# Kernel optimization log

Measured on AMD Instinct MI355X. Metric: run time of the kernel, lower is better.

Reference implementation:

```python
import jax, jax.numpy as jnp
import numpy as np

B, S, D = 4, 2048, 1024

def setup_inputs() -> dict:
    key = jax.random.key(0)
    k1, k2, k3, k4 = jax.random.split(key, 4)
    scale = 1.0 / np.sqrt(D)
    return {
        "x": jax.random.normal(k1, (B, S, D), dtype=jnp.float32),
        "Wq": jax.random.normal(k2, (D, D), dtype=jnp.float32) * scale,
        "Wk": jax.random.normal(k3, (D, D), dtype=jnp.float32) * scale,
        "Wv": jax.random.normal(k4, (D, D), dtype=jnp.float32) * scale,
    }

def reference(x, Wq, Wk, Wv):
    # Q, K, V projections: [B, S, D] @ [D, D]
    Q = jnp.einsum("bsd,de->bse", x, Wq)
    Kp = jnp.einsum("bsd,de->bse", x, Wk)
    V = jnp.einsum("bsd,de->bse", x, Wv)
    # scores: [B, S, S] -- NOTE: original module applies NO 1/sqrt(d) scaling
    scores = jnp.einsum("bqd,bkd->bqk", Q, Kp)
    attn = jax.nn.softmax(scores, axis=-1)
    # context: [B, S, D]
    return jnp.einsum("bqk,bkd->bqd", attn, V)
```

## Files before the change

### kernel.cpp

```cpp
#include <hip/hip_runtime.h>
#include <hip/hip_bf16.h>

#define ATT_B 4
#define ATT_S 2048
#define ATT_D 1024

#define BM 128
#define BN 128
#define BK 32

typedef __attribute__((ext_vector_type(8))) short bf16x8;
typedef __attribute__((ext_vector_type(4))) float f32x4;

__device__ inline unsigned short f2bf_rne(float f) {
  unsigned u = __float_as_uint(f);
  u += 0x7FFFu + ((u >> 16) & 1u);
  return (unsigned short)(u >> 16);
}

__device__ inline void gll16(const void* g, void* l) {
  __builtin_amdgcn_global_load_lds(
      (const __attribute__((address_space(1))) void*)g,
      (__attribute__((address_space(3))) void*)l, 16, 0, 0);
}

template<int NT, int AMODE, int OMODE>
__global__ __launch_bounds__(256, 2)
void gemm_bt(const void* __restrict__ Apv, const void* __restrict__ Alv,
             const unsigned short* __restrict__ Bh,
             const unsigned short* __restrict__ Bl,
             void* __restrict__ C0, void* __restrict__ C1,
             int K, int pitchA, int pitchB, int pitchC, int mtiles_pb,
             size_t Abstride, size_t Bbstride, size_t Cbstride)
{
  __shared__ unsigned short sAh[BM * BK];
  __shared__ unsigned short sBh[BN * BK];
  __shared__ unsigned short sAl[(NT == 3) ? BM * BK : 8];
  __shared__ unsigned short sBl[(NT == 3) ? BN * BK : 8];

  const int tid  = threadIdx.x;
  const int wave = tid >> 6;
  const int lane = tid & 63;
  const int l16  = lane & 15;
  const int lh   = lane >> 4;
  const int wm   = wave >> 1;
  const int wn   = wave & 1;

  const int bt   = blockIdx.y / mtiles_pb;
  const int ml   = blockIdx.y % mtiles_pb;
  const int row0 = ml * BM;
  const int col0 = blockIdx.x * BN;

  const unsigned short* Bhb = Bh + (size_t)bt * Bbstride;
  const unsigned short* Blb = (NT == 3) ? (Bl + (size_t)bt * Bbstride) : (const unsigned short*)nullptr;

  const unsigned short* Ahb = nullptr;
  const unsigned short* Alb = nullptr;
  const float*          Af  = nullptr;
  if (AMODE == 0) {
    Ahb = (const unsigned short*)Apv + (size_t)bt * Abstride;
    if (NT == 3) Alb = (const unsigned short*)Alv + (size_t)bt * Abstride;
  } else {
    Af = (const float*)Apv + (size_t)bt * Abstride;
  }

  f32x4 acc[4][4] = {};

  for (int k0 = 0; k0 < K; k0 += BK) {
#pragma unroll
    for (int j = 0; j < 2; ++j) {
      const int off = tid * 16 + j * 4096;
      const int r   = off >> 6;
      const int kb  = off & 63;
      const char* g = (const char*)Bhb + ((size_t)(col0 + r) * pitchB + k0) * 2 + kb;
      char* l = (char*)sBh + (wave << 10) + j * 4096;
      gll16(g, l);
    }
    if (NT == 3) {
#pragma unroll
      for (int j = 0; j < 2; ++j) {
        const int off = tid * 16 + j * 4096;
        const int r   = off >> 6;
        const int kb  = off & 63;
        const char* g = (const char*)Blb + ((size_t)(col0 + r) * pitchB + k0) * 2 + kb;
        char* l = (char*)sBl + (wave << 10) + j * 4096;
        gll16(g, l);
      }
    }

    if (AMODE == 0) {
#pragma unroll
      for (int j = 0; j < 2; ++j) {
        const int off = tid * 16 + j * 4096;
        const int r   = off >> 6;
        const int kb  = off & 63;
        const char* g = (const char*)Ahb + ((size_t)(row0 + r) * pitchA + k0) * 2 + kb;
        char* l = (char*)sAh + (wave << 10) + j * 4096;
        gll16(g, l);
      }
      if (NT == 3) {
#pragma unroll
        for (int j = 0; j < 2; ++j) {
          const int off = tid * 16 + j * 4096;
          const int r   = off >> 6;
          const int kb  = off & 63;
          const char* g = (const char*)Alb + ((size_t)(row0 + r) * pitchA + k0) * 2 + kb;
          char* l = (char*)sAl + (wave << 10) + j * 4096;
          gll16(g, l);
        }
      }
    } else {
#pragma unroll
      for (int j = 0; j < 4; ++j) {
        const int lin4 = tid + j * 256;
        const int r    = lin4 >> 3;
        const int c4   = lin4 & 7;
        const float4 v = *(const float4*)(Af + (size_t)(row0 + r) * pitchA + k0 + c4 * 4);
        const unsigned ux = __float_as_uint(v.x), uy = __float_as_uint(v.y);
        const unsigned uz = __float_as_uint(v.z), uw = __float_as_uint(v.w);
        ushort4 hi;
        hi.x = (unsigned short)(ux >> 16); hi.y = (unsigned short)(uy >> 16);
        hi.z = (unsigned short)(uz >> 16); hi.w = (unsigned short)(uw >> 16);
        *(ushort4*)&sAh[r * BK + c4 * 4] = hi;
        if (NT == 3) {
          ushort4 lo;
          lo.x = f2bf_rne(v.x - __uint_as_float(ux & 0xFFFF0000u));
          lo.y = f2bf_rne(v.y - __uint_as_float(uy & 0xFFFF0000u));
          lo.z = f2bf_rne(v.z - __uint_as_float(uz & 0xFFFF0000u));
          lo.w = f2bf_rne(v.w - __uint_as_float(uw & 0xFFFF0000u));
          *(ushort4*)&sAl[r * BK + c4 * 4] = lo;
        }
      }
    }
    __syncthreads();

    bf16x8 ah[4], bh4[4], al[4], bl4[4];
#pragma unroll
    for (int t = 0; t < 4; ++t) {
      ah[t]  = *(const bf16x8*)&sAh[(wm * 64 + t * 16 + l16) * BK + lh * 8];
      bh4[t] = *(const bf16x8*)&sBh[(wn * 64 + t * 16 + l16) * BK + lh * 8];
      if (NT == 3) {
        al[t]  = *(const bf16x8*)&sAl[(wm * 64 + t * 16 + l16) * BK + lh * 8];
        bl4[t] = *(const bf16x8*)&sBl[(wn * 64 + t * 16 + l16) * BK + lh * 8];
      }
    }
#pragma unroll
    for (int i = 0; i < 4; ++i)
#pragma unroll
      for (int j = 0; j < 4; ++j) {
        f32x4 c = acc[i][j];
        if (NT == 3) {
          c = __builtin_amdgcn_mfma_f32_16x16x32_bf16(al[i], bh4[j], c, 0, 0, 0);
          c = __builtin_amdgcn_mfma_f32_16x16x32_bf16(ah[i], bl4[j], c, 0, 0, 0);
        }
        c = __builtin_amdgcn_mfma_f32_16x16x32_bf16(ah[i], bh4[j], c, 0, 0, 0);
        acc[i][j] = c;
      }
    __syncthreads();
  }

#pragma unroll
  for (int i = 0; i < 4; ++i) {
    const int mBase = row0 + wm * 64 + i * 16 + lh * 4;
#pragma unroll
    for (int j = 0; j < 4; ++j) {
      const int n = col0 + wn * 64 + j * 16 + l16;
      if (OMODE == 0) {
        float* C = (float*)C0 + (size_t)bt * Cbstride;
#pragma unroll
        for (int r = 0; r < 4; ++r)
          C[(size_t)(mBase + r) * pitchC + n] = acc[i][j][r];
      } else if (OMODE == 1) {
        unsigned short* Ch = (unsigned short*)C0;
        unsigned short* Cl = (unsigned short*)C1;
#pragma unroll
        for (int r = 0; r < 4; ++r) {
          const float f = acc[i][j][r];
          const unsigned u = __float_as_uint(f);
          Ch[(size_t)(mBase + r) * pitchC + n] = (unsigned short)(u >> 16);
          Cl[(size_t)(mBase + r) * pitchC + n] =
              f2bf_rne(f - __uint_as_float(u & 0xFFFF0000u));
        }
      } else {
        unsigned short* Vt = (unsigned short*)C0;
        const int b2 = mBase >> 11;
        const int sr = mBase & 2047;
        ushort4 o;
        o.x = f2bf_rne(acc[i][j][0]); o.y = f2bf_rne(acc[i][j][1]);
        o.z = f2bf_rne(acc[i][j][2]); o.w = f2bf_rne(acc[i][j][3]);
        *(ushort4*)&Vt[(size_t)b2 * (1024u * 2048u) + (size_t)n * 2048 + sr] = o;
      }
    }
  }
}

__global__ __launch_bounds__(256)
void wsplit(const float* __restrict__ W, unsigned short* __restrict__ Wh,
            unsigned short* __restrict__ Wl) {
  __shared__ float t[32][33];
  const int k0 = blockIdx.x * 32;
  const int n0 = blockIdx.y * 32;
  const int tx = threadIdx.x & 31;
  const int ty = threadIdx.x >> 5;
#pragma unroll
  for (int i = 0; i < 32; i += 8)
    t[ty + i][tx] = W[(size_t)(k0 + ty + i) * 1024 + (n0 + tx)];
  __syncthreads();
#pragma unroll
  for (int i = 0; i < 32; i += 8) {
    const float f = t[tx][ty + i];
    const unsigned u = __float_as_uint(f);
    Wh[(size_t)(n0 + ty + i) * 1024 + (k0 + tx)] = (unsigned short)(u >> 16);
    Wl[(size_t)(n0 + ty + i) * 1024 + (k0 + tx)] =
        f2bf_rne(f - __uint_as_float(u & 0xFFFF0000u));
  }
}

__global__ __launch_bounds__(256)
void softmax_inplace(float* __restrict__ S) {
  const int wave = threadIdx.x >> 6;
  const int lane = threadIdx.x & 63;
  float* rp = S + ((size_t)blockIdx.x * 4 + wave) * 2048;

  float4 v[8];
#pragma unroll
  for (int i = 0; i < 8; ++i) v[i] = *(const float4*)&rp[lane * 4 + i * 256];

  float m = -1e30f;
#pragma unroll
  for (int i = 0; i < 8; ++i)
    m = fmaxf(m, fmaxf(fmaxf(v[i].x, v[i].y), fmaxf(v[i].z, v[i].w)));
#pragma unroll
  for (int s = 32; s; s >>= 1) m = fmaxf(m, __shfl_xor(m, s));

  float sum = 0.f;
#pragma unroll
  for (int i = 0; i < 8; ++i) {
    v[i].x = __expf(v[i].x - m); v[i].y = __expf(v[i].y - m);
    v[i].z = __expf(v[i].z - m); v[i].w = __expf(v[i].w - m);
    sum += (v[i].x + v[i].y) + (v[i].z + v[i].w);
  }
#pragma unroll
  for (int s = 32; s; s >>= 1) sum += __shfl_xor(sum, s);
  const float inv = 1.0f / sum;

  unsigned short* pp = (unsigned short*)rp;
#pragma unroll
  for (int i = 0; i < 8; ++i) {
    ushort4 o;
    o.x = f2bf_rne(v[i].x * inv); o.y = f2bf_rne(v[i].y * inv);
    o.z = f2bf_rne(v[i].z * inv); o.w = f2bf_rne(v[i].w * inv);
    *(ushort4*)&pp[lane * 4 + i * 256] = o;
  }
}

extern "C" void kernel_launch(void* const* d_in, const int* in_sizes, int n_in,
                              void* d_out, int out_size, void* d_ws, size_t ws_size,
                              hipStream_t stream) {
  const float* x  = (const float*)d_in[0];
  const float* Wq = (const float*)d_in[1];
  const float* Wk = (const float*)d_in[2];
  const float* Wv = (const float*)d_in[3];
  float* out = (float*)d_out;

  char* ws = (char*)d_ws;
  const size_t MB = 1024 * 1024;
  unsigned short* Qh = (unsigned short*)(ws + 0 * MB);
  unsigned short* Ql = (unsigned short*)(ws + 16 * MB);
  unsigned short* Kh = (unsigned short*)(ws + 32 * MB);
  unsigned short* Kl = (unsigned short*)(ws + 48 * MB);
  unsigned short* Vt = (unsigned short*)(ws + 64 * MB);
  char* R = ws + 80 * MB;
  unsigned short* Wqh = (unsigned short*)(R + 0 * MB);
  unsigned short* Wql = (unsigned short*)(R + 2 * MB);
  unsigned short* Wkh = (unsigned short*)(R + 4 * MB);
  unsigned short* Wkl = (unsigned short*)(R + 6 * MB);
  unsigned short* Wvh = (unsigned short*)(R + 8 * MB);
  unsigned short* Wvl = (unsigned short*)(R + 10 * MB);
  float* Sbuf = (float*)R;

  const size_t avail = (ws_size > 80 * MB) ? (ws_size - 80 * MB) : 0;
  int h = 128;
  const int cands[4] = {2048, 1024, 512, 256};
  for (int c = 0; c < 4; ++c) {
    if ((size_t)4 * cands[c] * 2048 * 4 <= avail) { h = cands[c]; break; }
  }

  dim3 gw(32, 32);
  wsplit<<<gw, 256, 0, stream>>>(Wq, Wqh, Wql);
  wsplit<<<gw, 256, 0, stream>>>(Wk, Wkh, Wkl);
  wsplit<<<gw, 256, 0, stream>>>(Wv, Wvh, Wvl);

  dim3 g1(ATT_D / BN, (ATT_B * ATT_S) / BM);
  gemm_bt<3, 1, 1><<<g1, 256, 0, stream>>>(x, nullptr, Wqh, Wql, Qh, Ql,
      1024, 1024, 1024, 1024, 64, 0, 0, 0);
  gemm_bt<3, 1, 1><<<g1, 256, 0, stream>>>(x, nullptr, Wkh, Wkl, Kh, Kl,
      1024, 1024, 1024, 1024, 64, 0, 0, 0);
  gemm_bt<1, 1, 2><<<g1, 256, 0, stream>>>(x, nullptr, Wvh, nullptr, Vt, nullptr,
      1024, 1024, 1024, 0, 64, 0, 0, 0);

  const int np = ATT_S / h;
  for (int p = 0; p < np; ++p) {
    const unsigned short* Ap  = Qh + (size_t)p * h * 1024;
    const unsigned short* Alp = Ql + (size_t)p * h * 1024;
    dim3 gs(ATT_S / BN, ATT_B * h / BM);
    gemm_bt<3, 0, 0><<<gs, 256, 0, stream>>>(Ap, Alp, Kh, Kl, Sbuf, nullptr,
        1024, 1024, 1024, 2048, h / 128,
        (size_t)ATT_S * 1024, (size_t)ATT_S * 1024, (size_t)h * 2048);
    softmax_inplace<<<dim3(ATT_B * h / 4), 256, 0, stream>>>(Sbuf);
    dim3 gp(ATT_D / BN, ATT_B * h / BM);
    gemm_bt<1, 0, 0><<<gp, 256, 0, stream>>>((const unsigned short*)Sbuf, nullptr,
        Vt, nullptr, out + (size_t)p * h * 1024, nullptr,
        2048, 4096, 2048, 1024, h / 128,
        (size_t)h * 4096, (size_t)1024 * 2048, (size_t)ATT_S * 1024);
  }
}
```

Baseline: 431.5 us.

## Add pipelined 256x256 split-bf16 GEMM for fused QK projection and scores

Introduces a new 512-thread GEMM kernel with 256x256 tiles, double-buffered global-to-LDS loads, an XOR-swizzled LDS layout, staggered waitcnt/barrier phases and a workgroup swizzle for L2 locality. The three bf16 split terms are handled as a concatenated K loop. Q and K projections are fused into one launch by concatenating Wq and Wk, and x is pre-split into hi/lo bf16 by a new kernel. The aim is higher MFMA utilisation and fewer launches for the 3-term projections and the QK^T scores. In exchange it uses 128KB of dynamic LDS with occupancy limits, extra workspace for Xh/Xl, and delicate hand-tuned vmcnt counts that must match the exact load issue order.

```diff
diff --git a/kernel.cpp b/kernel.cpp
--- a/kernel.cpp
+++ b/kernel.cpp
@@ -11,6 +11,7 @@
 
 typedef __attribute__((ext_vector_type(8))) short bf16x8;
 typedef __attribute__((ext_vector_type(4))) float f32x4;
+typedef unsigned short ushort_t;
 
 __device__ inline unsigned short f2bf_rne(float f) {
   unsigned u = __float_as_uint(f);
@@ -24,19 +25,197 @@
       (__attribute__((address_space(3))) void*)l, 16, 0, 0);
 }
 
+__device__ __forceinline__ void vwait(int sel) {
+  if (sel == 0)      asm volatile("s_waitcnt vmcnt(6)" ::: "memory");
+  else if (sel == 1) asm volatile("s_waitcnt vmcnt(4)" ::: "memory");
+  else               asm volatile("s_waitcnt vmcnt(0)" ::: "memory");
+}
+
+template<int NTERM, int OM>
+__global__ __launch_bounds__(512, 2)
+void gemm256(const ushort_t* __restrict__ Ah, const ushort_t* __restrict__ Al,
+             const ushort_t* __restrict__ Bh, const ushort_t* __restrict__ Bl,
+             void* __restrict__ C0, void* __restrict__ C1,
+             void* __restrict__ C2, void* __restrict__ C3,
+             int NT0, int pitchA, int pitchB, int pitchC, int mtiles_pb,
+             size_t AbStride, size_t BbStride, size_t CbStride)
+{
+  extern __shared__ char lds[];
+  const int tid  = threadIdx.x;
+  const int wave = tid >> 6, lane = tid & 63;
+  const int l16  = lane & 15, lh = lane >> 4;
+  const int wm   = wave >> 2;
+  const int wn   = wave & 3;
+
+  const int bid = blockIdx.x + gridDim.x * blockIdx.y;
+  const int nwg = gridDim.x * gridDim.y;
+  const int swz = (bid & 7) * (nwg >> 3) + (bid >> 3);
+  const int bx  = swz % gridDim.x;
+  const int by  = swz / gridDim.x;
+
+  const int bt   = by / mtiles_pb;
+  const int row0 = (by % mtiles_pb) * 256;
+  const int col0 = bx * 256;
+
+  const ushort_t* Ahb = Ah + (size_t)bt * AbStride;
+  const ushort_t* Alb = (NTERM == 3) ? (Al + (size_t)bt * AbStride) : nullptr;
+  const ushort_t* Bhb = Bh + (size_t)bt * BbStride;
+  const ushort_t* Blb = (NTERM == 3) ? (Bl + (size_t)bt * BbStride) : nullptr;
+
+  const int NT = NTERM * NT0;
+
+  auto srcs = [&](int t, const ushort_t*& As, const ushort_t*& Bs, int& koff) {
+    int seg = 0;
+    if (NTERM == 3) seg = (t >= 2 * NT0) ? 2 : ((t >= NT0) ? 1 : 0);
+    koff = (t - seg * NT0) * 64;
+    As = (NTERM == 3 && seg == 1) ? Alb : Ahb;
+    Bs = (NTERM == 3 && seg == 2) ? Blb : Bhb;
+  };
+
+  auto stage = [&](const ushort_t* src, int rowbase, int pitch, int koff,
+                   int kh, int op, int p) {
+#pragma unroll
+    for (int c = 0; c < 2; ++c) {
+      const int chunk = wave + c * 8;
+      const int o  = chunk * 1024 + lane * 16;
+      const int os = o ^ (((o >> 7) & 3) << 4);
+      const int row  = os >> 6;
+      const int colb = os & 63;
+      const char* g = (const char*)src +
+          ((size_t)(rowbase + row) * pitch + koff + kh * 32) * 2 + colb;
+      gll16(g, lds + op * 65536 + p * 32768 + kh * 16384 + chunk * 1024);
+    }
+  };
+
+  auto ldA = [&](int p, int ks, int row) -> bf16x8 {
+    int local = row * 64 + lh * 16;
+    local ^= ((local >> 7) & 3) << 4;
+    return *(const bf16x8*)(lds + p * 32768 + ks * 16384 + local);
+  };
+  auto ldB = [&](int p, int ks, int row) -> bf16x8 {
+    int local = row * 64 + lh * 16;
+    local ^= ((local >> 7) & 3) << 4;
+    return *(const bf16x8*)(lds + 65536 + p * 32768 + ks * 16384 + local);
+  };
+
+  f32x4 acc[8][4] = {};
+
+  {
+    const ushort_t *As, *Bs; int ko;
+    srcs(0, As, Bs, ko);
+    stage(As, row0, pitchA, ko, 0, 0, 0);
+    stage(Bs, col0, pitchB, ko, 0, 1, 0);
+    stage(As, row0, pitchA, ko, 1, 0, 0);
+    stage(Bs, col0, pitchB, ko, 1, 1, 0);
+    srcs(1, As, Bs, ko);
+    stage(As, row0, pitchA, ko, 0, 0, 1);
+    stage(Bs, col0, pitchB, ko, 0, 1, 1);
+    asm volatile("s_waitcnt vmcnt(8)" ::: "memory");
+    __builtin_amdgcn_s_barrier();
+  }
+
+  auto mma16 = [&](bf16x8 (&a)[4], bf16x8 (&b)[4], int mh) {
+    __builtin_amdgcn_s_setprio(1);
+#pragma unroll
+    for (int mf = 0; mf < 4; ++mf)
+#pragma unroll
+      for (int nf = 0; nf < 4; ++nf)
+        acc[mh * 4 + mf][nf] = __builtin_amdgcn_mfma_f32_16x16x32_bf16(
+            a[mf], b[nf], acc[mh * 4 + mf][nf], 0, 0, 0);
+    __builtin_amdgcn_s_setprio(0);
+  };
+
+  for (int t = 0; t < NT; ++t) {
+    const int p    = t & 1;
+    const int vsel = (t < NT - 2) ? 0 : ((t == NT - 2) ? 1 : 2);
+    const ushort_t *As1, *Bs1, *As2, *Bs2; int ko1, ko2;
+    srcs(t + 1, As1, Bs1, ko1);
+    srcs(t + 2, As2, Bs2, ko2);
+    const bool st1 = (t + 1 < NT), st2 = (t + 2 < NT);
+
+    bf16x8 a[4], b[4];
+
+#pragma unroll
+    for (int f = 0; f < 4; ++f) a[f] = ldA(p, 0, wm * 128 + f * 16 + l16);
+#pragma unroll
+    for (int f = 0; f < 4; ++f) b[f] = ldB(p, 0, wn * 64 + f * 16 + l16);
+    if (st1) stage(As1, row0, pitchA, ko1, 1, 0, p ^ 1);
+    vwait(vsel); __builtin_amdgcn_s_barrier();
+    asm volatile("s_waitcnt lgkmcnt(0)" ::: "memory");
+    __builtin_amdgcn_sched_barrier(0);
+    mma16(a, b, 0);
+    __builtin_amdgcn_s_barrier();
+
+#pragma unroll
+    for (int f = 0; f < 4; ++f) a[f] = ldA(p, 0, wm * 128 + 64 + f * 16 + l16);
+    if (st1) stage(Bs1, col0, pitchB, ko1, 1, 1, p ^ 1);
+    vwait(vsel); __builtin_amdgcn_s_barrier();
+    asm volatile("s_waitcnt lgkmcnt(0)" ::: "memory");
+    __builtin_amdgcn_sched_barrier(0);
+    mma16(a, b, 1);
+    __builtin_amdgcn_s_barrier();
+
+#pragma unroll
+    for (int f = 0; f < 4; ++f) a[f] = ldA(p, 1, wm * 128 + f * 16 + l16);
+#pragma unroll
+    for (int f = 0; f < 4; ++f) b[f] = ldB(p, 1, wn * 64 + f * 16 + l16);
+    if (st2) stage(As2, row0, pitchA, ko2, 0, 0, p);
+    vwait(vsel); __builtin_amdgcn_s_barrier();
+    asm volatile("s_waitcnt lgkmcnt(0)" ::: "memory");
+    __builtin_amdgcn_sched_barrier(0);
+    mma16(a, b, 0);
+    __builtin_amdgcn_s_barrier();
+
+#pragma unroll
+    for (int f = 0; f < 4; ++f) a[f] = ldA(p, 1, wm * 128 + 64 + f * 16 + l16);
+    if (st2) stage(Bs2, col0, pitchB, ko2, 0, 1, p);
+    vwait(vsel); __builtin_amdgcn_s_barrier();
+    asm volatile("s_waitcnt lgkmcnt(0)" ::: "memory");
+    __builtin_amdgcn_sched_barrier(0);
+    mma16(a, b, 1);
+    __builtin_amdgcn_s_barrier();
+  }
+
+#pragma unroll
+  for (int i = 0; i < 8; ++i) {
+    const int mBase = row0 + wm * 128 + (i >> 2) * 64 + (i & 3) * 16 + lh * 4;
+#pragma unroll
+    for (int nf = 0; nf < 4; ++nf) {
+      const int n = col0 + wn * 64 + nf * 16 + l16;
+      if (OM == 0) {
+        float* Cb = (float*)C0 + (size_t)bt * CbStride;
+#pragma unroll
+        for (int r = 0; r < 4; ++r)
+          Cb[(size_t)(mBase + r) * pitchC + n] = acc[i][nf][r];
+      } else {
+        ushort_t* Dh = (ushort_t*)((col0 < 1024) ? C0 : C2);
+        ushort_t* Dl = (ushort_t*)((col0 < 1024) ? C1 : C3);
+        const int nn = (col0 < 1024) ? n : (n - 1024);
+#pragma unroll
+        for (int r = 0; r < 4; ++r) {
+          const float f = acc[i][nf][r];
+          const unsigned u = __float_as_uint(f);
+          Dh[(size_t)(mBase + r) * pitchC + nn] = (ushort_t)(u >> 16);
+          Dl[(size_t)(mBase + r) * pitchC + nn] =
+              f2bf_rne(f - __uint_as_float(u & 0xFFFF0000u));
+        }
+      }
+    }
+  }
+}
+
 template<int NT, int AMODE, int OMODE>
 __global__ __launch_bounds__(256, 2)
 void gemm_bt(const void* __restrict__ Apv, const void* __restrict__ Alv,
-             const unsigned short* __restrict__ Bh,
-             const unsigned short* __restrict__ Bl,
+             const ushort_t* __restrict__ Bh, const ushort_t* __restrict__ Bl,
              void* __restrict__ C0, void* __restrict__ C1,
              int K, int pitchA, int pitchB, int pitchC, int mtiles_pb,
              size_t Abstride, size_t Bbstride, size_t Cbstride)
 {
-  __shared__ unsigned short sAh[BM * BK];
-  __shared__ unsigned short sBh[BN * BK];
-  __shared__ unsigned short sAl[(NT == 3) ? BM * BK : 8];
-  __shared__ unsigned short sBl[(NT == 3) ? BN * BK : 8];
+  __shared__ ushort_t sAh[BM * BK];
+  __shared__ ushort_t sBh[BN * BK];
+  __shared__ ushort_t sAl[(NT == 3) ? BM * BK : 8];
+  __shared__ ushort_t sBl[(NT == 3) ? BN * BK : 8];
 
   const int tid  = threadIdx.x;
   const int wave = tid >> 6;
@@ -51,15 +230,15 @@
   const int row0 = ml * BM;
   const int col0 = blockIdx.x * BN;
 
-  const unsigned short* Bhb = Bh + (size_t)bt * Bbstride;
-  const unsigned short* Blb = (NT == 3) ? (Bl + (size_t)bt * Bbstride) : (const unsigned short*)nullptr;
-
-  const unsigned short* Ahb = nullptr;
-  const unsigned short* Alb = nullptr;
-  const float*          Af  = nullptr;
+  const ushort_t* Bhb = Bh + (size_t)bt * Bbstride;
+  const ushort_t* Blb = (NT == 3) ? (Bl + (size_t)bt * Bbstride) : nullptr;
+
+  const ushort_t* Ahb = nullptr;
+  const ushort_t* Alb = nullptr;
+  const float*    Af  = nullptr;
   if (AMODE == 0) {
-    Ahb = (const unsigned short*)Apv + (size_t)bt * Abstride;
-    if (NT == 3) Alb = (const unsigned short*)Alv + (size_t)bt * Abstride;
+    Ahb = (const ushort_t*)Apv + (size_t)bt * Abstride;
+    if (NT == 3) Alb = (const ushort_t*)Alv + (size_t)bt * Abstride;
   } else {
     Af = (const float*)Apv + (size_t)bt * Abstride;
   }
@@ -73,21 +252,8 @@
       const int r   = off >> 6;
       const int kb  = off & 63;
       const char* g = (const char*)Bhb + ((size_t)(col0 + r) * pitchB + k0) * 2 + kb;
-      char* l = (char*)sBh + (wave << 10) + j * 4096;
-      gll16(g, l);
-    }
-    if (NT == 3) {
-#pragma unroll
-      for (int j = 0; j < 2; ++j) {
-        const int off = tid * 16 + j * 4096;
-        const int r   = off >> 6;
-        const int kb  = off & 63;
-        const char* g = (const char*)Blb + ((size_t)(col0 + r) * pitchB + k0) * 2 + kb;
-        char* l = (char*)sBl + (wave << 10) + j * 4096;
-        gll16(g, l);
-      }
-    }
-
+      gll16(g, (char*)sBh + (wave << 10) + j * 4096);
+    }
     if (AMODE == 0) {
 #pragma unroll
       for (int j = 0; j < 2; ++j) {
@@ -95,19 +261,7 @@
         const int r   = off >> 6;
         const int kb  = off & 63;
         const char* g = (const char*)Ahb + ((size_t)(row0 + r) * pitchA + k0) * 2 + kb;
-        char* l = (char*)sAh + (wave << 10) + j * 4096;
-        gll16(g, l);
-      }
-      if (NT == 3) {
-#pragma unroll
-        for (int j = 0; j < 2; ++j) {
-          const int off = tid * 16 + j * 4096;
-          const int r   = off >> 6;
-          const int kb  = off & 63;
-          const char* g = (const char*)Alb + ((size_t)(row0 + r) * pitchA + k0) * 2 + kb;
-          char* l = (char*)sAl + (wave << 10) + j * 4096;
-          gll16(g, l);
-        }
+        gll16(g, (char*)sAh + (wave << 10) + j * 4096);
       }
     } else {
 #pragma unroll
@@ -119,43 +273,24 @@
         const unsigned ux = __float_as_uint(v.x), uy = __float_as_uint(v.y);
         const unsigned uz = __float_as_uint(v.z), uw = __float_as_uint(v.w);
         ushort4 hi;
-        hi.x = (unsigned short)(ux >> 16); hi.y = (unsigned short)(uy >> 16);
-        hi.z = (unsigned short)(uz >> 16); hi.w = (unsigned short)(uw >> 16);
+        hi.x = (ushort_t)(ux >> 16); hi.y = (ushort_t)(uy >> 16);
+        hi.z = (ushort_t)(uz >> 16); hi.w = (ushort_t)(uw >> 16);
         *(ushort4*)&sAh[r * BK + c4 * 4] = hi;
-        if (NT == 3) {
-          ushort4 lo;
-          lo.x = f2bf_rne(v.x - __uint_as_float(ux & 0xFFFF0000u));
-          lo.y = f2bf_rne(v.y - __uint_as_float(uy & 0xFFFF0000u));
-          lo.z = f2bf_rne(v.z - __uint_as_float(uz & 0xFFFF0000u));
-          lo.w = f2bf_rne(v.w - __uint_as_float(uw & 0xFFFF0000u));
-          *(ushort4*)&sAl[r * BK + c4 * 4] = lo;
-        }
       }
     }
     __syncthreads();
 
-    bf16x8 ah[4], bh4[4], al[4], bl4[4];
+    bf16x8 ah[4], bh4[4];
 #pragma unroll
     for (int t = 0; t < 4; ++t) {
       ah[t]  = *(const bf16x8*)&sAh[(wm * 64 + t * 16 + l16) * BK + lh * 8];
       bh4[t] = *(const bf16x8*)&sBh[(wn * 64 + t * 16 + l16) * BK + lh * 8];
-      if (NT == 3) {
-        al[t]  = *(const bf16x8*)&sAl[(wm * 64 + t * 16 + l16) * BK + lh * 8];
-        bl4[t] = *(const bf16x8*)&sBl[(wn * 64 + t * 16 + l16) * BK + lh * 8];
-      }
     }
 #pragma unroll
     for (int i = 0; i < 4; ++i)
 #pragma unroll
-      for (int j = 0; j < 4; ++j) {
-        f32x4 c = acc[i][j];
-        if (NT == 3) {
-          c = __builtin_amdgcn_mfma_f32_16x16x32_bf16(al[i], bh4[j], c, 0, 0, 0);
-          c = __builtin_amdgcn_mfma_f32_16x16x32_bf16(ah[i], bl4[j], c, 0, 0, 0);
-        }
-        c = __builtin_amdgcn_mfma_f32_16x16x32_bf16(ah[i], bh4[j], c, 0, 0, 0);
-        acc[i][j] = c;
-      }
+      for (int j = 0; j < 4; ++j)
+        acc[i][j] = __builtin_amdgcn_mfma_f32_16x16x32_bf16(ah[i], bh4[j], acc[i][j], 0, 0, 0);
     __syncthreads();
   }
 
@@ -170,19 +305,8 @@
 #pragma unroll
         for (int r = 0; r < 4; ++r)
           C[(size_t)(mBase + r) * pitchC + n] = acc[i][j][r];
-      } else if (OMODE == 1) {
-        unsigned short* Ch = (unsigned short*)C0;
-        unsigned short* Cl = (unsigned short*)C1;
-#pragma unroll
-        for (int r = 0; r < 4; ++r) {
-          const float f = acc[i][j][r];
-          const unsigned u = __float_as_uint(f);
-          Ch[(size_t)(mBase + r) * pitchC + n] = (unsigned short)(u >> 16);
-          Cl[(size_t)(mBase + r) * pitchC + n] =
-              f2bf_rne(f - __uint_as_float(u & 0xFFFF0000u));
-        }
       } else {
-        unsigned short* Vt = (unsigned short*)C0;
+        ushort_t* Vt = (ushort_t*)C0;
         const int b2 = mBase >> 11;
         const int sr = mBase & 2047;
         ushort4 o;
@@ -195,8 +319,8 @@
 }
 
 __global__ __launch_bounds__(256)
-void wsplit(const float* __restrict__ W, unsigned short* __restrict__ Wh,
-            unsigned short* __restrict__ Wl) {
+void wsplit(const float* __restrict__ W, ushort_t* __restrict__ Wh,
+            ushort_t* __restrict__ Wl) {
   __shared__ float t[32][33];
   const int k0 = blockIdx.x * 32;
   const int n0 = blockIdx.y * 32;
@@ -210,9 +334,30 @@
   for (int i = 0; i < 32; i += 8) {
     const float f = t[tx][ty + i];
     const unsigned u = __float_as_uint(f);
-    Wh[(size_t)(n0 + ty + i) * 1024 + (k0 + tx)] = (unsigned short)(u >> 16);
+    Wh[(size_t)(n0 + ty + i) * 1024 + (k0 + tx)] = (ushort_t)(u >> 16);
     Wl[(size_t)(n0 + ty + i) * 1024 + (k0 + tx)] =
         f2bf_rne(f - __uint_as_float(u & 0xFFFF0000u));
+  }
+}
+
+__global__ __launch_bounds__(256)
+void xsplit(const float* __restrict__ x, ushort_t* __restrict__ Xh,
+            ushort_t* __restrict__ Xl) {
+  const size_t i0 = ((size_t)blockIdx.x * 256 + threadIdx.x) * 16;
+#pragma unroll
+  for (int j = 0; j < 4; ++j) {
+    const float4 v = *(const float4*)(x + i0 + j * 4);
+    const unsigned ux = __float_as_uint(v.x), uy = __float_as_uint(v.y);
+    const unsigned uz = __float_as_uint(v.z), uw = __float_as_uint(v.w);
+    ushort4 hi, lo;
+    hi.x = (ushort_t)(ux >> 16); hi.y = (ushort_t)(uy >> 16);
+    hi.z = (ushort_t)(uz >> 16); hi.w = (ushort_t)(uw >> 16);
+    lo.x = f2bf_rne(v.x - __uint_as_float(ux & 0xFFFF0000u));
+    lo.y = f2bf_rne(v.y - __uint_as_float(uy & 0xFFFF0000u));
+    lo.z = f2bf_rne(v.z - __uint_as_float(uz & 0xFFFF0000u));
+    lo.w = f2bf_rne(v.w - __uint_as_float(uw & 0xFFFF0000u));
+    *(ushort4*)(Xh + i0 + j * 4) = hi;
+    *(ushort4*)(Xl + i0 + j * 4) = lo;
   }
 }
 
@@ -244,7 +389,7 @@
   for (int s = 32; s; s >>= 1) sum += __shfl_xor(sum, s);
   const float inv = 1.0f / sum;
 
-  unsigned short* pp = (unsigned short*)rp;
+  ushort_t* pp = (ushort_t*)rp;
 #pragma unroll
   for (int i = 0; i < 8; ++i) {
     ushort4 o;
@@ -265,52 +410,50 @@
 
   char* ws = (char*)d_ws;
   const size_t MB = 1024 * 1024;
-  unsigned short* Qh = (unsigned short*)(ws + 0 * MB);
-  unsigned short* Ql = (unsigned short*)(ws + 16 * MB);
-  unsigned short* Kh = (unsigned short*)(ws + 32 * MB);
-  unsigned short* Kl = (unsigned short*)(ws + 48 * MB);
-  unsigned short* Vt = (unsigned short*)(ws + 64 * MB);
-  char* R = ws + 80 * MB;
-  unsigned short* Wqh = (unsigned short*)(R + 0 * MB);
-  unsigned short* Wql = (unsigned short*)(R + 2 * MB);
-  unsigned short* Wkh = (unsigned short*)(R + 4 * MB);
-  unsigned short* Wkl = (unsigned short*)(R + 6 * MB);
-  unsigned short* Wvh = (unsigned short*)(R + 8 * MB);
-  unsigned short* Wvl = (unsigned short*)(R + 10 * MB);
-  float* Sbuf = (float*)R;
+  ushort_t* Qh = (ushort_t*)(ws +  0 * MB);
+  ushort_t* Ql = (ushort_t*)(ws + 16 * MB);
+  ushort_t* Kh = (ushort_t*)(ws + 32 * MB);
+  ushort_t* Kl = (ushort_t*)(ws + 48 * MB);
+  ushort_t* Vt = (ushort_t*)(ws + 64 * MB);
+  ushort_t* Xh   = (ushort_t*)(ws +  80 * MB);
+  ushort_t* Xl   = (ushort_t*)(ws +  96 * MB);
+  ushort_t* Wqkh = (ushort_t*)(ws + 112 * MB);
+  ushort_t* Wqkl = (ushort_t*)(ws + 116 * MB);
+  ushort_t* Wvh  = (ushort_t*)(ws + 120 * MB);
+  ushort_t* Wvl  = (ushort_t*)(ws + 122 * MB);
+  float* Sbuf = (float*)(ws + 80 * MB);
 
   const size_t avail = (ws_size > 80 * MB) ? (ws_size - 80 * MB) : 0;
-  int h = 128;
+  int h = 256;
   const int cands[4] = {2048, 1024, 512, 256};
-  for (int c = 0; c < 4; ++c) {
+  for (int c = 0; c < 4; ++c)
     if ((size_t)4 * cands[c] * 2048 * 4 <= avail) { h = cands[c]; break; }
-  }
 
   dim3 gw(32, 32);
-  wsplit<<<gw, 256, 0, stream>>>(Wq, Wqh, Wql);
-  wsplit<<<gw, 256, 0, stream>>>(Wk, Wkh, Wkl);
+  wsplit<<<gw, 256, 0, stream>>>(Wq, Wqkh, Wqkl);
+  wsplit<<<gw, 256, 0, stream>>>(Wk, Wqkh + 1024 * 1024, Wqkl + 1024 * 1024);
   wsplit<<<gw, 256, 0, stream>>>(Wv, Wvh, Wvl);
-
-  dim3 g1(ATT_D / BN, (ATT_B * ATT_S) / BM);
-  gemm_bt<3, 1, 1><<<g1, 256, 0, stream>>>(x, nullptr, Wqh, Wql, Qh, Ql,
-      1024, 1024, 1024, 1024, 64, 0, 0, 0);
-  gemm_bt<3, 1, 1><<<g1, 256, 0, stream>>>(x, nullptr, Wkh, Wkl, Kh, Kl,
-      1024, 1024, 1024, 1024, 64, 0, 0, 0);
-  gemm_bt<1, 1, 2><<<g1, 256, 0, stream>>>(x, nullptr, Wvh, nullptr, Vt, nullptr,
+  xsplit<<<2048, 256, 0, stream>>>(x, Xh, Xl);
+
+  gemm256<3, 1><<<dim3(8, 32), 512, 131072, stream>>>(
+      Xh, Xl, Wqkh, Wqkl, Qh, Ql, Kh, Kl,
+      16, 1024, 1024, 1024, 32, 0, 0, 0);
+
+  gemm_bt<1, 1, 2><<<dim3(8, 64), 256, 0, stream>>>(
+      x, nullptr, Wvh, nullptr, Vt, nullptr,
       1024, 1024, 1024, 0, 64, 0, 0, 0);
 
   const int np = ATT_S / h;
   for (int p = 0; p < np; ++p) {
-    const unsigned short* Ap  = Qh + (size_t)p * h * 1024;
-    const unsigned short* Alp = Ql + (size_t)p * h * 1024;
-    dim3 gs(ATT_S / BN, ATT_B * h / BM);
-    gemm_bt<3, 0, 0><<<gs, 256, 0, stream>>>(Ap, Alp, Kh, Kl, Sbuf, nullptr,
-        1024, 1024, 1024, 2048, h / 128,
+    gemm256<3, 0><<<dim3(8, ATT_B * h / 256), 512, 131072, stream>>>(
+        Qh + (size_t)p * h * 1024, Ql + (size_t)p * h * 1024, Kh, Kl,
+        Sbuf, nullptr, nullptr, nullptr,
+        16, 1024, 1024, 2048, h / 256,
         (size_t)ATT_S * 1024, (size_t)ATT_S * 1024, (size_t)h * 2048);
     softmax_inplace<<<dim3(ATT_B * h / 4), 256, 0, stream>>>(Sbuf);
-    dim3 gp(ATT_D / BN, ATT_B * h / BM);
-    gemm_bt<1, 0, 0><<<gp, 256, 0, stream>>>((const unsigned short*)Sbuf, nullptr,
-        Vt, nullptr, out + (size_t)p * h * 1024, nullptr,
+    gemm_bt<1, 0, 0><<<dim3(8, ATT_B * h / 128), 256, 0, stream>>>(
+        (const ushort_t*)Sbuf, nullptr, Vt, nullptr,
+        out + (size_t)p * h * 1024, nullptr,
         2048, 4096, 2048, 1024, h / 128,
         (size_t)h * 4096, (size_t)1024 * 2048, (size_t)ATT_S * 1024);
   }
```

Measured after the change: 419.9 us. 2.7% less time.
